# Performance work log

Hardware: AMD Instinct MI355X
Metric: run time of the kernel (lower is better)

Reference implementation:

```python
import jax, jax.numpy as jnp
import numpy as np
from jax import lax

_F1 = np.array([1., 3., 3., 1.], dtype=np.float32)
_F1 = _F1 / _F1.sum()
F2D = jnp.asarray(np.outer(_F1, _F1))  # [4,4] normalized FIR filter
LRELU_GAIN = float(np.sqrt(2.0))


def _upfirdn2d_up(x, up, pad0, pad1, gain):
    # zero-insertion upsample + pad + FIR filter (VALID depthwise conv)
    B, C, H, W = x.shape
    if up > 1:
        x = jnp.zeros((B, C, H, up, W, up), x.dtype).at[:, :, :, 0, :, 0].set(x)
        x = x.reshape(B, C, H * up, W * up)
    x = jnp.pad(x, ((0, 0), (0, 0), (pad0, pad1), (pad0, pad1)))
    k = jnp.broadcast_to((F2D * gain).astype(x.dtype), (C, 1, 4, 4))
    return lax.conv_general_dilated(x, k, (1, 1), 'VALID', feature_group_count=C)


def _affine(w, aw, ab):
    # FullyConnectedLayer: weight_gain = 1/sqrt(in_features), bias_init handled in setup
    return w @ aw.T * (1.0 / np.sqrt(aw.shape[1])) + ab


def _mod_conv(x, weight, styles, up):
    # fused modulated conv2d with demodulation, batch-as-groups trick
    B = x.shape[0]
    O, I, kh, kw = weight.shape
    w = weight[None] * styles[:, None, :, None, None]          # [B,O,I,kh,kw]
    d = lax.rsqrt(jnp.sum(jnp.square(w), axis=(2, 3, 4)) + 1e-8)  # [B,O]
    w = w * d[:, :, None, None, None]
    if up == 2:
        # conv2d_resample: FIR upsample (gain=up^2), then true conv (flipped weight)
        # padding=1, fw=4, up=2 -> px0 = 1 + (4+2-1)//2 = 3, px1 = 1 + (4-2)//2 = 2
        x = _upfirdn2d_up(x, 2, 3, 2, 4.0)
        w = w[:, :, :, ::-1, ::-1]
        pad = 'VALID'
    else:
        pad = ((kh // 2, kh // 2), (kw // 2, kw // 2))
    xr = x.reshape(1, B * I, x.shape[2], x.shape[3])
    wr = w.reshape(B * O, I, kh, kw)
    y = lax.conv_general_dilated(xr, wr, (1, 1), pad, feature_group_count=B)
    return y.reshape(B, O, y.shape[2], y.shape[3])


def _lrelu_bias(x, b, clamp=256.0):
    # bias_act: lrelu(x+b) * sqrt(2), clamp
    x = x + b[None, :, None, None]
    x = jnp.where(x >= 0, x, 0.2 * x) * LRELU_GAIN
    return jnp.clip(x, -clamp, clamp)


def setup_inputs() -> dict:
    key = jax.random.key(0)
    ks = jax.random.split(key, 12)
    B, Cin, Cout, Wd, R, IC = 8, 512, 512, 512, 64, 3
    r = R // 2
    return dict(
        x=jax.random.normal(ks[0], (B, Cin, r, r), jnp.float32),
        img=jax.random.normal(ks[1], (B, IC, r, r), jnp.float32),
        ws=jax.random.normal(ks[2], (B, 3, Wd), jnp.float32),
        a0_w=jax.random.normal(ks[3], (Cin, Wd), jnp.float32),
        a0_b=jnp.ones((Cin,), jnp.float32),
        w0=jax.random.normal(ks[4], (Cout, Cin, 3, 3), jnp.float32),
        b0=jnp.zeros((Cout,), jnp.float32),
        ns0=jnp.asarray(0.1, jnp.float32),
        nc0=jax.random.normal(ks[5], (R, R), jnp.float32),
        a1_w=jax.random.normal(ks[6], (Cout, Wd), jnp.float32),
        a1_b=jnp.ones((Cout,), jnp.float32),
        w1=jax.random.normal(ks[7], (Cout, Cout, 3, 3), jnp.float32),
        b1=jnp.zeros((Cout,), jnp.float32),
        ns1=jnp.asarray(0.1, jnp.float32),
        nc1=jax.random.normal(ks[8], (R, R), jnp.float32),
        at_w=jax.random.normal(ks[9], (Cout, Wd), jnp.float32),
        at_b=jnp.ones((Cout,), jnp.float32),
        wt=jax.random.normal(ks[10], (IC, Cout), jnp.float32),
        bt=jnp.zeros((IC,), jnp.float32),
    )


def reference(x, img, ws, a0_w, a0_b, w0, b0, ns0, nc0,
              a1_w, a1_b, w1, b1, ns1, nc1, at_w, at_b, wt, bt):
    # conv0: modulated conv, up=2, const noise, lrelu bias-act with clamp
    s0 = _affine(ws[:, 0], a0_w, a0_b)
    h = _mod_conv(x, w0, s0, up=2)
    h = h + nc0[None, None] * ns0
    h = _lrelu_bias(h, b0)
    # conv1: modulated conv, up=1
    s1 = _affine(ws[:, 1], a1_w, a1_b)
    h = _mod_conv(h, w1, s1, up=1)
    h = h + nc1[None, None] * ns1
    h = _lrelu_bias(h, b1)
    # skip architecture: upsample img (upsample2d: px0=2, px1=1, gain=4)
    img_up = _upfirdn2d_up(img, 2, 2, 1, 4.0)
    # torgb: 1x1 modulated conv, no demodulation, styles scaled by weight_gain
    st = _affine(ws[:, 2], at_w, at_b) * (1.0 / np.sqrt(wt.shape[1]))
    y = jnp.einsum('bihw,bi,oi->bohw', h, st, wt)
    y = jnp.clip(y + bt[None, :, None, None], -256.0, 256.0)
    return h, img_up + y
```

## Files before the change

### kernel.cpp

```cpp
#include <hip/hip_runtime.h>
#include <stdint.h>

typedef unsigned short u16;
typedef unsigned int   u32;

#define DEVINL __device__ __forceinline__

typedef __bf16 bf16x8 __attribute__((ext_vector_type(8)));
typedef float  f32x4  __attribute__((ext_vector_type(4)));
typedef unsigned short u16x8 __attribute__((ext_vector_type(8)));

#define RSQRT512 0.044194173824159216f
#define LRELU_G  1.4142135623730951f

DEVINL u16 f2bf(float f) {
  union { float f; u32 u; } v; v.f = f;
  u32 r = v.u + 0x7fffu + ((v.u >> 16) & 1u);
  return (u16)(r >> 16);
}
DEVINL float bf2f(u16 b) {
  union { u32 u; float f; } v; v.u = ((u32)b) << 16;
  return v.f;
}

#define AS1 __attribute__((address_space(1)))
#define AS3 __attribute__((address_space(3)))
DEVINL void gload16(const void* g, void* l) {
  __builtin_amdgcn_global_load_lds((AS1 const u32*)(uintptr_t)g,
                                   (AS3 u32*)(u32)(uintptr_t)l, 16, 0, 0);
}

__global__ __launch_bounds__(256)
void style_kernel(const float* __restrict__ wsin,
                  const float* __restrict__ a0w, const float* __restrict__ a0b,
                  const float* __restrict__ a1w, const float* __restrict__ a1b,
                  const float* __restrict__ atw, const float* __restrict__ atb,
                  float* __restrict__ s_all)
{
  int wid = threadIdx.x >> 6, lane = threadIdx.x & 63;
  int idx = blockIdx.x * 4 + wid;
  int j = idx >> 12;
  int b = (idx >> 9) & 7;
  int o = idx & 511;
  const float* A  = (j == 0) ? a0w : ((j == 1) ? a1w : atw);
  const float* Ab = (j == 0) ? a0b : ((j == 1) ? a1b : atb);
  const float* wv = wsin + (b * 3 + j) * 512;
  float p = 0.f;
  #pragma unroll
  for (int m = 0; m < 512; m += 64) p += wv[m + lane] * A[(size_t)o * 512 + m + lane];
  #pragma unroll
  for (int s = 32; s; s >>= 1) p += __shfl_xor(p, s, 64);
  if (lane == 0) {
    float v = p * RSQRT512 + Ab[o];
    if (j == 2) v *= RSQRT512;
    s_all[idx] = v;
  }
}

__global__ __launch_bounds__(256)
void demod_kernel(const float* __restrict__ w, const float* __restrict__ s_j,
                  float* __restrict__ dOut)
{
  int o = blockIdx.x;
  int t = threadIdx.x;
  __shared__ float red2[4][8];
  float part[8];
  #pragma unroll
  for (int b = 0; b < 8; ++b) part[b] = 0.f;
  #pragma unroll
  for (int hh = 0; hh < 2; ++hh) {
    int i = t + hh * 256;
    const float* wp = w + ((size_t)o * 512 + i) * 9;
    float ws = 0.f;
    #pragma unroll
    for (int k = 0; k < 9; ++k) ws += wp[k] * wp[k];
    #pragma unroll
    for (int b = 0; b < 8; ++b) {
      float sv = s_j[b * 512 + i];
      part[b] += sv * sv * ws;
    }
  }
  #pragma unroll
  for (int b = 0; b < 8; ++b)
    #pragma unroll
    for (int s = 32; s; s >>= 1) part[b] += __shfl_xor(part[b], s, 64);
  int wid = t >> 6, lane = t & 63;
  if (lane == 0) {
    #pragma unroll
    for (int b = 0; b < 8; ++b) red2[wid][b] = part[b];
  }
  __syncthreads();
  if (t < 8) {
    float d = red2[0][t] + red2[1][t] + red2[2][t] + red2[3][t];
    dOut[t * 512 + o] = 1.0f / sqrtf(d + 1e-8f);
  }
}

template <int FLIP>
__global__ __launch_bounds__(256)
void wpack_kernel(const float* __restrict__ w, const float* __restrict__ s_j,
                  const float* __restrict__ dIn, u16* __restrict__ wg)
{
  int b = blockIdx.x >> 6;
  int kq = blockIdx.x & 63;
  float sv[8];
  #pragma unroll
  for (int e = 0; e < 8; ++e) sv[e] = s_j[b * 512 + kq * 8 + e];
  int t = threadIdx.x;
  #pragma unroll 1
  for (int rep = 0; rep < 2; ++rep) {
    int o = rep * 256 + t;
    float d = dIn[b * 512 + o];
    const float* wp = w + ((size_t)o * 512 + kq * 8) * 9;
    float wv[72];
    #pragma unroll
    for (int j = 0; j < 72; ++j) wv[j] = wp[j];
    #pragma unroll
    for (int tapOut = 0; tapOut < 9; ++tapOut) {
      int ksrc = FLIP ? (8 - tapOut) : tapOut;
      u16x8 g;
      #pragma unroll
      for (int e = 0; e < 8; ++e) g[e] = f2bf(wv[e * 9 + ksrc] * sv[e] * d);
      *(u16x8*)&wg[((((size_t)(b * 9 + tapOut)) * 64 + kq) * 512 + o) * 8] = g;
    }
  }
}

__global__ __launch_bounds__(256)
void upblur_kernel(const float* __restrict__ x, u16* __restrict__ xb)
{
  int b = blockIdx.x >> 6, c8 = blockIdx.x & 63;
  __shared__ float slab[8192];
  int t = threadIdx.x;
  const float* sp = x + (((size_t)(b * 512 + c8 * 8)) << 10);
  #pragma unroll
  for (int i = 0; i < 32; ++i) slab[t + i * 256] = sp[t + i * 256];
  __syncthreads();
  u16* ob = xb + ((size_t)(b * 64 + c8)) * 34848;
  #pragma unroll 1
  for (int idx = t; idx < 4356; idx += 256) {
    int p = idx / 66;
    int q = idx - p * 66;
    int m0, m1; float wy0, wy1;
    if ((p & 1) == 0) { m0 = (p >> 1) - 1; wy0 = 0.75f; m1 = p >> 1;       wy1 = 0.25f; }
    else              { m0 = (p - 3) >> 1; wy0 = 0.25f; m1 = (p - 1) >> 1; wy1 = 0.75f; }
    int n0, n1; float wx0, wx1;
    if ((q & 1) == 0) { n0 = (q >> 1) - 1; wx0 = 0.75f; n1 = q >> 1;       wx1 = 0.25f; }
    else              { n0 = (q - 3) >> 1; wx0 = 0.25f; n1 = (q - 1) >> 1; wx1 = 0.75f; }
    bool vm0 = (unsigned)m0 < 32u, vm1 = (unsigned)m1 < 32u;
    bool vn0 = (unsigned)n0 < 32u, vn1 = (unsigned)n1 < 32u;
    float w00 = (vm0 & vn0) ? wy0 * wx0 : 0.f;
    float w01 = (vm0 & vn1) ? wy0 * wx1 : 0.f;
    float w10 = (vm1 & vn0) ? wy1 * wx0 : 0.f;
    float w11 = (vm1 & vn1) ? wy1 * wx1 : 0.f;
    int i00 = ((m0 & 31) << 5) + (n0 & 31);
    int i01 = ((m0 & 31) << 5) + (n1 & 31);
    int i10 = ((m1 & 31) << 5) + (n0 & 31);
    int i11 = ((m1 & 31) << 5) + (n1 & 31);
    u16x8 g;
    #pragma unroll
    for (int e = 0; e < 8; ++e) {
      const float* se = slab + (e << 10);
      float a = w00 * se[i00] + w01 * se[i01] + w10 * se[i10] + w11 * se[i11];
      g[e] = f2bf(a);
    }
    *(u16x8*)&ob[idx * 8] = g;
  }
}

__global__ __launch_bounds__(256)
void ringzero_kernel(u16* __restrict__ hp)
{
  u16* obase = hp + (size_t)blockIdx.x * 34848;
  int t = threadIdx.x;
  if (t < 260) {
    int y, x;
    if (t < 66)       { y = 0;       x = t; }
    else if (t < 132) { y = 65;      x = t - 66; }
    else if (t < 196) { y = t - 131; x = 0; }
    else              { y = t - 195; x = 65; }
    u16x8 z = {0, 0, 0, 0, 0, 0, 0, 0};
    *(u16x8*)&obase[(y * 66 + x) * 8] = z;
  }
}

extern __shared__ u16 dynLds[];

template <int EPI>
__global__ __launch_bounds__(512, 4)
void conv8(const u16* __restrict__ xin,
           const u16* __restrict__ wg,
           const float* __restrict__ noise,
           const float* __restrict__ nsp,
           const float* __restrict__ bias,
           u16* __restrict__ hpOut,
           float* __restrict__ hOut)
{
  int blk = (blockIdx.x & 7) * 64 + (blockIdx.x >> 3);
  int b  = blk >> 6;
  int ot = (blk >> 5) & 1;
  int pt = blk & 31;
  int o0 = ot << 8;
  int y0 = pt << 1;

  int t = threadIdx.x;
  int w = t >> 6;
  int lane = t & 63;
  int gq = lane >> 4, r = lane & 15;
  int w2 = w >> 2;
  int w4 = w & 3;

  u16* Wl = dynLds;
  u16* Xl = dynLds + 16384;

  f32x4 acc[4][4];
  #pragma unroll
  for (int i = 0; i < 4; ++i)
    #pragma unroll
    for (int j = 0; j < 4; ++j) acc[i][j] = (f32x4){0.f, 0.f, 0.f, 0.f};

  const u16* wbB = wg + (size_t)b * 2359296;
  const u16* xbB = xin + (size_t)b * 2230272;

  auto STAGE = [&](int tile, int pb) {
    int tap = tile >> 4;
    int ck  = tile & 15;
    int dy = (tap * 171) >> 9;
    int dx = tap - dy * 3;
    #pragma unroll
    for (int q = 0; q < 3; ++q) {
      int m = q * 8 + w;
      if (m < 16) {
        int j = m & 3, rbo = m >> 2;
        const u16* src = wbB + ((size_t)(tap * 64 + ck * 4 + j)) * 4096
                             + ((size_t)o0 + rbo * 64 + lane) * 8;
        gload16(src, Wl + pb * 8192 + j * 2048 + rbo * 512);
      } else {
        int n = m - 16;
        int j = n & 3, rbx = n >> 2;
        const u16* src = xbB + (size_t)(ck * 4 + j) * 34848
                             + (((size_t)(y0 + rbx + dy) * 66) + dx + lane) * 8;
        gload16(src, Xl + pb * 4096 + j * 1024 + rbx * 512);
      }
    }
  };

  auto TILE = [&](int pb) {
    bf16x8 af[4], bfr[4];
    if constexpr (EPI == 0) {
      #pragma unroll
      for (int f = 0; f < 4; ++f) {
        af[f]  = *(const bf16x8*)&Xl[pb * 4096 + gq * 1024 + ((w2 * 64 + f * 16 + r) << 3)];
        bfr[f] = *(const bf16x8*)&Wl[pb * 8192 + gq * 2048 + ((w4 * 64 + f * 16 + r) << 3)];
      }
    } else {
      #pragma unroll
      for (int f = 0; f < 4; ++f) {
        af[f]  = *(const bf16x8*)&Wl[pb * 8192 + gq * 2048 + ((w4 * 64 + f * 16 + r) << 3)];
        bfr[f] = *(const bf16x8*)&Xl[pb * 4096 + gq * 1024 + ((w2 * 64 + f * 16 + r) << 3)];
      }
    }
    __builtin_amdgcn_s_setprio(1);
    #pragma unroll
    for (int fa = 0; fa < 4; ++fa)
      #pragma unroll
      for (int fb = 0; fb < 4; ++fb)
        acc[fa][fb] = __builtin_amdgcn_mfma_f32_16x16x32_bf16(af[fa], bfr[fb], acc[fa][fb], 0, 0, 0);
    __builtin_amdgcn_s_setprio(0);
  };

  STAGE(0, 0);
  STAGE(1, 1);
  asm volatile("s_waitcnt vmcnt(3)" ::: "memory");
  __builtin_amdgcn_sched_barrier(0);
  __builtin_amdgcn_s_barrier();
  __builtin_amdgcn_sched_barrier(0);

  int p = 0;
  #pragma unroll 1
  for (int tl = 0; tl < 144; ++tl) {
    TILE(p);
    __builtin_amdgcn_sched_barrier(0);
    __builtin_amdgcn_s_barrier();
    __builtin_amdgcn_sched_barrier(0);
    if (tl < 142) {
      STAGE(tl + 2, p);
      asm volatile("s_waitcnt vmcnt(3)" ::: "memory");
    } else if (tl == 142) {
      asm volatile("s_waitcnt vmcnt(0)" ::: "memory");
    }
    __builtin_amdgcn_sched_barrier(0);
    __builtin_amdgcn_s_barrier();
    __builtin_amdgcn_sched_barrier(0);
    p ^= 1;
  }
  __builtin_amdgcn_sched_barrier(0);

  float ns = nsp[0];
  if constexpr (EPI == 0) {
    #pragma unroll
    for (int fa = 0; fa < 4; ++fa) {
      #pragma unroll
      for (int fb = 0; fb < 4; ++fb) {
        int oo = o0 + w4 * 64 + fb * 16 + r;
        float bo = bias[oo];
        #pragma unroll
        for (int v = 0; v < 4; ++v) {
          int px = w2 * 64 + fa * 16 + gq * 4 + v;
          int pg = (pt << 7) + px;
          int y = pg >> 6, x2 = pg & 63;
          float val = acc[fa][fb][v] + noise[pg] * ns + bo;
          val = (val >= 0.f ? val : 0.2f * val) * LRELU_G;
          val = fminf(fmaxf(val, -256.f), 256.f);
          hpOut[((((size_t)b * 64 + (oo >> 3)) * 66 + (y + 1)) * 66 + (x2 + 1)) * 8 + (oo & 7)] = f2bf(val);
        }
      }
    }
  } else {
    #pragma unroll
    for (int fa = 0; fa < 4; ++fa) {
      #pragma unroll
      for (int fb = 0; fb < 4; ++fb) {
        int px = w2 * 64 + fb * 16 + r;
        int pg = (pt << 7) + px;
        float nv = noise[pg] * ns;
        #pragma unroll
        for (int v = 0; v < 4; ++v) {
          int oo = o0 + w4 * 64 + fa * 16 + gq * 4 + v;
          float val = acc[fa][fb][v] + nv + bias[oo];
          val = (val >= 0.f ? val : 0.2f * val) * LRELU_G;
          val = fminf(fmaxf(val, -256.f), 256.f);
          hOut[((size_t)(b * 512 + oo) << 12) + pg] = val;
        }
      }
    }
  }
}

__global__ __launch_bounds__(256)
void torgb_kernel(const float* __restrict__ h, const float* __restrict__ s_all,
                  const float* __restrict__ wt, const float* __restrict__ bt,
                  const float* __restrict__ img, float* __restrict__ out2)
{
  int b = blockIdx.x >> 4;
  int y = ((blockIdx.x & 15) << 2) + (threadIdx.x >> 6);
  int x = threadIdx.x & 63;
  __shared__ float stw[3][512];
  const float* st = s_all + 2 * 4096 + b * 512;
  for (int i = threadIdx.x; i < 512; i += 256) {
    float s = st[i];
    stw[0][i] = s * wt[i];
    stw[1][i] = s * wt[512 + i];
    stw[2][i] = s * wt[1024 + i];
  }
  __syncthreads();
  const float* hp = h + ((size_t)b * 512 << 12) + (y << 6) + x;
  float a0 = 0.f, a1 = 0.f, a2 = 0.f;
  #pragma unroll 8
  for (int i = 0; i < 512; ++i) {
    float v = hp[(size_t)i << 12];
    a0 += v * stw[0][i]; a1 += v * stw[1][i]; a2 += v * stw[2][i];
  }
  float accs[3] = {a0, a1, a2};
  int my0, my1; float wy0, wy1;
  if ((y & 1) == 0) { my0 = (y >> 1) - 1; wy0 = 0.25f; my1 = y >> 1;       wy1 = 0.75f; }
  else              { my0 = y >> 1;       wy0 = 0.75f; my1 = (y >> 1) + 1; wy1 = 0.25f; }
  int mx0, mx1; float wx0, wx1;
  if ((x & 1) == 0) { mx0 = (x >> 1) - 1; wx0 = 0.25f; mx1 = x >> 1;       wx1 = 0.75f; }
  else              { mx0 = x >> 1;       wx0 = 0.75f; mx1 = (x >> 1) + 1; wx1 = 0.25f; }
  bool vy0 = (unsigned)my0 < 32u, vy1 = (unsigned)my1 < 32u;
  bool vx0 = (unsigned)mx0 < 32u, vx1 = (unsigned)mx1 < 32u;
  #pragma unroll
  for (int o = 0; o < 3; ++o) {
    float yv = fminf(fmaxf(accs[o] + bt[o], -256.f), 256.f);
    const float* ib = img + ((size_t)(b * 3 + o) << 10);
    float iu = 0.f;
    if (vy0 & vx0) iu += wy0 * wx0 * ib[(my0 << 5) + mx0];
    if (vy0 & vx1) iu += wy0 * wx1 * ib[(my0 << 5) + mx1];
    if (vy1 & vx0) iu += wy1 * wx0 * ib[(my1 << 5) + mx0];
    if (vy1 & vx1) iu += wy1 * wx1 * ib[(my1 << 5) + mx1];
    out2[((size_t)(b * 3 + o) << 12) + (y << 6) + x] = iu + yv;
  }
}

extern "C" void kernel_launch(void* const* d_in, const int* in_sizes, int n_in,
                              void* d_out, int out_size, void* d_ws, size_t ws_size,
                              hipStream_t stream) {
  (void)in_sizes; (void)n_in; (void)out_size; (void)ws_size;
  const float* x   = (const float*)d_in[0];
  const float* img = (const float*)d_in[1];
  const float* ws_ = (const float*)d_in[2];
  const float* a0w = (const float*)d_in[3];
  const float* a0b = (const float*)d_in[4];
  const float* w0  = (const float*)d_in[5];
  const float* b0  = (const float*)d_in[6];
  const float* ns0 = (const float*)d_in[7];
  const float* nc0 = (const float*)d_in[8];
  const float* a1w = (const float*)d_in[9];
  const float* a1b = (const float*)d_in[10];
  const float* w1  = (const float*)d_in[11];
  const float* b1  = (const float*)d_in[12];
  const float* ns1 = (const float*)d_in[13];
  const float* nc1 = (const float*)d_in[14];
  const float* atw = (const float*)d_in[15];
  const float* atb = (const float*)d_in[16];
  const float* wt  = (const float*)d_in[17];
  const float* bt  = (const float*)d_in[18];

  char* wsp = (char*)d_ws;
  float* s_all = (float*)wsp;
  u16* wg0 = (u16*)(wsp + 49152);
  u16* wg1 = (u16*)(wsp + 49152 + 37748736ull);
  u16* xb  = (u16*)(wsp + 49152 + 2ull * 37748736);
  u16* hp  = (u16*)(wsp + 49152 + 2ull * 37748736 + 35684352);
  float* d0 = (float*)(wsp + 49152 + 2ull * 37748736 + 2ull * 35684352);
  float* d1 = (float*)(wsp + 49152 + 2ull * 37748736 + 2ull * 35684352 + 16384);

  float* h_out = (float*)d_out;
  float* out2  = (float*)d_out + 16777216;

  (void)hipFuncSetAttribute((const void*)conv8<0>,
                            hipFuncAttributeMaxDynamicSharedMemorySize, 49152);
  (void)hipFuncSetAttribute((const void*)conv8<1>,
                            hipFuncAttributeMaxDynamicSharedMemorySize, 49152);

  style_kernel<<<3072, 256, 0, stream>>>(ws_, a0w, a0b, a1w, a1b, atw, atb, s_all);
  demod_kernel<<<512, 256, 0, stream>>>(w0, s_all, d0);
  demod_kernel<<<512, 256, 0, stream>>>(w1, s_all + 4096, d1);
  wpack_kernel<1><<<512, 256, 0, stream>>>(w0, s_all, d0, wg0);
  wpack_kernel<0><<<512, 256, 0, stream>>>(w1, s_all + 4096, d1, wg1);
  upblur_kernel<<<512, 256, 0, stream>>>(x, xb);
  ringzero_kernel<<<512, 256, 0, stream>>>(hp);
  conv8<0><<<512, 512, 49152, stream>>>(xb, wg0, nc0, ns0, b0, hp, nullptr);
  conv8<1><<<512, 512, 49152, stream>>>(hp, wg1, nc1, ns1, b1, nullptr, h_out);
  torgb_kernel<<<128, 256, 0, stream>>>(h_out, s_all, wt, bt, img, out2);
}
```

Measured before the change: 380.0 us.

## Load activation fragments directly into registers, staging only weights through LDS

```diff
diff --git a/kernel.cpp b/kernel.cpp
--- a/kernel.cpp
+++ b/kernel.cpp
@@ -187,7 +187,7 @@
 extern __shared__ u16 dynLds[];
 
 template <int EPI>
-__global__ __launch_bounds__(512, 4)
+__global__ __launch_bounds__(512, 2)
 void conv8(const u16* __restrict__ xin,
            const u16* __restrict__ wg,
            const float* __restrict__ noise,
@@ -211,7 +211,6 @@
   int w4 = w & 3;
 
   u16* Wl = dynLds;
-  u16* Xl = dynLds + 16384;
 
   f32x4 acc[4][4];
   #pragma unroll
@@ -222,79 +221,80 @@
   const u16* wbB = wg + (size_t)b * 2359296;
   const u16* xbB = xin + (size_t)b * 2230272;
 
-  auto STAGE = [&](int tile, int pb) {
+  auto STAGEW = [&](int tile, int pb) {
+    int tap = tile >> 4;
+    int ck  = tile & 15;
+    #pragma unroll
+    for (int q = 0; q < 2; ++q) {
+      int m = q * 8 + w;
+      int j = m & 3, rb = m >> 2;
+      const u16* src = wbB + ((size_t)(tap * 64 + ck * 4 + j)) * 4096
+                           + ((size_t)o0 + rb * 64 + lane) * 8;
+      gload16(src, Wl + pb * 8192 + j * 2048 + rb * 512);
+    }
+  };
+
+  auto LOADX = [&](int tile, bf16x8 (&xf)[4]) {
     int tap = tile >> 4;
     int ck  = tile & 15;
     int dy = (tap * 171) >> 9;
     int dx = tap - dy * 3;
-    #pragma unroll
-    for (int q = 0; q < 3; ++q) {
-      int m = q * 8 + w;
-      if (m < 16) {
-        int j = m & 3, rbo = m >> 2;
-        const u16* src = wbB + ((size_t)(tap * 64 + ck * 4 + j)) * 4096
-                             + ((size_t)o0 + rbo * 64 + lane) * 8;
-        gload16(src, Wl + pb * 8192 + j * 2048 + rbo * 512);
-      } else {
-        int n = m - 16;
-        int j = n & 3, rbx = n >> 2;
-        const u16* src = xbB + (size_t)(ck * 4 + j) * 34848
-                             + (((size_t)(y0 + rbx + dy) * 66) + dx + lane) * 8;
-        gload16(src, Xl + pb * 4096 + j * 1024 + rbx * 512);
-      }
-    }
+    const u16* base = xbB + (size_t)(ck * 4 + gq) * 34848
+                          + (((size_t)(y0 + w2 + dy)) * 66 + dx) * 8;
+    #pragma unroll
+    for (int f = 0; f < 4; ++f)
+      xf[f] = *(const bf16x8*)(base + (size_t)(f * 16 + r) * 8);
   };
 
-  auto TILE = [&](int pb) {
-    bf16x8 af[4], bfr[4];
-    if constexpr (EPI == 0) {
-      #pragma unroll
-      for (int f = 0; f < 4; ++f) {
-        af[f]  = *(const bf16x8*)&Xl[pb * 4096 + gq * 1024 + ((w2 * 64 + f * 16 + r) << 3)];
-        bfr[f] = *(const bf16x8*)&Wl[pb * 8192 + gq * 2048 + ((w4 * 64 + f * 16 + r) << 3)];
-      }
-    } else {
-      #pragma unroll
-      for (int f = 0; f < 4; ++f) {
-        af[f]  = *(const bf16x8*)&Wl[pb * 8192 + gq * 2048 + ((w4 * 64 + f * 16 + r) << 3)];
-        bfr[f] = *(const bf16x8*)&Xl[pb * 4096 + gq * 1024 + ((w2 * 64 + f * 16 + r) << 3)];
-      }
-    }
+  auto TILE = [&](int pb, bf16x8 (&xf)[4]) {
+    bf16x8 wf[4];
+    #pragma unroll
+    for (int f = 0; f < 4; ++f)
+      wf[f] = *(const bf16x8*)&Wl[pb * 8192 + gq * 2048 + ((w4 * 64 + f * 16 + r) << 3)];
     __builtin_amdgcn_s_setprio(1);
     #pragma unroll
     for (int fa = 0; fa < 4; ++fa)
       #pragma unroll
-      for (int fb = 0; fb < 4; ++fb)
-        acc[fa][fb] = __builtin_amdgcn_mfma_f32_16x16x32_bf16(af[fa], bfr[fb], acc[fa][fb], 0, 0, 0);
+      for (int fb = 0; fb < 4; ++fb) {
+        if constexpr (EPI == 0)
+          acc[fa][fb] = __builtin_amdgcn_mfma_f32_16x16x32_bf16(xf[fa], wf[fb], acc[fa][fb], 0, 0, 0);
+        else
+          acc[fa][fb] = __builtin_amdgcn_mfma_f32_16x16x32_bf16(wf[fa], xf[fb], acc[fa][fb], 0, 0, 0);
+      }
     __builtin_amdgcn_s_setprio(0);
   };
 
-  STAGE(0, 0);
-  STAGE(1, 1);
-  asm volatile("s_waitcnt vmcnt(3)" ::: "memory");
+  auto BODY = [&](int tl, bf16x8 (&cur)[4], bf16x8 (&nxt)[4]) {
+    TILE(tl & 1, cur);
+    __builtin_amdgcn_sched_barrier(0);
+    __builtin_amdgcn_s_barrier();
+    __builtin_amdgcn_sched_barrier(0);
+    if (tl < 143) LOADX(tl + 1, nxt);
+    if (tl < 142) {
+      STAGEW(tl + 2, tl & 1);
+      asm volatile("s_waitcnt vmcnt(6)" ::: "memory");
+    } else if (tl == 142) {
+      asm volatile("s_waitcnt vmcnt(4)" ::: "memory");
+    }
+    __builtin_amdgcn_sched_barrier(0);
+    __builtin_amdgcn_s_barrier();
+    __builtin_amdgcn_sched_barrier(0);
+  };
+
+  bf16x8 xfA[4], xfB[4];
+  STAGEW(0, 0);
+  STAGEW(1, 1);
+  LOADX(0, xfA);
+  asm volatile("s_waitcnt vmcnt(0)" ::: "memory");
   __builtin_amdgcn_sched_barrier(0);
   __builtin_amdgcn_s_barrier();
   __builtin_amdgcn_sched_barrier(0);
 
-  int p = 0;
   #pragma unroll 1
-  for (int tl = 0; tl < 144; ++tl) {
-    TILE(p);
-    __builtin_amdgcn_sched_barrier(0);
-    __builtin_amdgcn_s_barrier();
-    __builtin_amdgcn_sched_barrier(0);
-    if (tl < 142) {
-      STAGE(tl + 2, p);
-      asm volatile("s_waitcnt vmcnt(3)" ::: "memory");
-    } else if (tl == 142) {
-      asm volatile("s_waitcnt vmcnt(0)" ::: "memory");
-    }
-    __builtin_amdgcn_sched_barrier(0);
-    __builtin_amdgcn_s_barrier();
-    __builtin_amdgcn_sched_barrier(0);
-    p ^= 1;
-  }
-  __builtin_amdgcn_sched_barrier(0);
+  for (int tl = 0; tl < 144; tl += 2) {
+    BODY(tl, xfA, xfB);
+    BODY(tl + 1, xfB, xfA);
+  }
 
   float ns = nsp[0];
   if constexpr (EPI == 0) {
@@ -420,9 +420,9 @@
   float* out2  = (float*)d_out + 16777216;
 
   (void)hipFuncSetAttribute((const void*)conv8<0>,
-                            hipFuncAttributeMaxDynamicSharedMemorySize, 49152);
+                            hipFuncAttributeMaxDynamicSharedMemorySize, 32768);
   (void)hipFuncSetAttribute((const void*)conv8<1>,
-                            hipFuncAttributeMaxDynamicSharedMemorySize, 49152);
+                            hipFuncAttributeMaxDynamicSharedMemorySize, 32768);
 
   style_kernel<<<3072, 256, 0, stream>>>(ws_, a0w, a0b, a1w, a1b, atw, atb, s_all);
   demod_kernel<<<512, 256, 0, stream>>>(w0, s_all, d0);
@@ -431,7 +431,7 @@
   wpack_kernel<0><<<512, 256, 0, stream>>>(w1, s_all + 4096, d1, wg1);
   upblur_kernel<<<512, 256, 0, stream>>>(x, xb);
   ringzero_kernel<<<512, 256, 0, stream>>>(hp);
-  conv8<0><<<512, 512, 49152, stream>>>(xb, wg0, nc0, ns0, b0, hp, nullptr);
-  conv8<1><<<512, 512, 49152, stream>>>(hp, wg1, nc1, ns1, b1, nullptr, h_out);
+  conv8<0><<<512, 512, 32768, stream>>>(xb, wg0, nc0, ns0, b0, hp, nullptr);
+  conv8<1><<<512, 512, 32768, stream>>>(hp, wg1, nc1, ns1, b1, nullptr, h_out);
   torgb_kernel<<<128, 256, 0, stream>>>(h_out, s_all, wt, bt, img, out2);
 }
```

After: 572.3 us. 1.51x slower.
